# Kernel tuning notes

Measured on AMD Instinct MI355X. Metric: run time of the kernel, lower is better.

## Reference

```python
import jax, jax.numpy as jnp
import numpy as np

B, S, CC, CF, E, H, NH = 16, 1024, 8, 8, 64, 1024, 16
DH = H // NH
VOCAB = 10000
EPS = 1e-5


def layer_norm(x, g, b):
    m = x.mean(-1, keepdims=True)
    v = x.var(-1, keepdims=True)
    return (x - m) / jnp.sqrt(v + EPS) * g + b


def setup_inputs():
    key = jax.random.key(0)
    ks = jax.random.split(key, 30)
    f32 = jnp.float32
    n = lambda k, shp, s=0.02: jax.random.normal(k, shp, f32) * s
    inp = {}
    inp['cate_x'] = jax.random.randint(ks[0], (B, S, CC), 0, VOCAB)
    inp['cont_x'] = jax.random.normal(ks[1], (B, S, CF), f32)
    inp['mask'] = jax.random.randint(ks[2], (B, S), 0, 2)
    # parameters
    inp['emb_table'] = n(ks[3], (VOCAB, E)).at[0].set(0.0)  # padding_idx=0
    inp['cate_W'] = n(ks[4], (CC * E, H)); inp['cate_b'] = jnp.zeros((H,), f32)
    inp['cate_ln_g'] = jnp.ones((H,), f32); inp['cate_ln_b'] = jnp.zeros((H,), f32)
    inp['bn_g'] = jnp.ones((CF,), f32); inp['bn_b'] = jnp.zeros((CF,), f32)
    inp['cont_W'] = n(ks[5], (CF, H)); inp['cont_b'] = jnp.zeros((H,), f32)
    inp['cont_ln_g'] = jnp.ones((H,), f32); inp['cont_ln_b'] = jnp.zeros((H,), f32)
    inp['comb_W'] = n(ks[6], (2 * H, H)); inp['comb_b'] = jnp.zeros((H,), f32)
    inp['comb_ln_g'] = jnp.ones((H,), f32); inp['comb_ln_b'] = jnp.zeros((H,), f32)
    inp['Wq'] = n(ks[7], (H, H)); inp['bq'] = jnp.zeros((H,), f32)
    inp['Wk'] = n(ks[8], (H, H)); inp['bk'] = jnp.zeros((H,), f32)
    inp['Wv'] = n(ks[9], (H, H)); inp['bv'] = jnp.zeros((H,), f32)
    inp['Wo'] = n(ks[10], (H, H)); inp['bo'] = jnp.zeros((H,), f32)
    return inp


def reference(cate_x, cont_x, mask, emb_table, cate_W, cate_b, cate_ln_g, cate_ln_b,
              bn_g, bn_b, cont_W, cont_b, cont_ln_g, cont_ln_b,
              comb_W, comb_b, comb_ln_g, comb_ln_b,
              Wq, bq, Wk, bk, Wv, bv, Wo, bo):
    # categorical path: embed -> flatten cols -> Linear+LN
    cate_emb = emb_table[cate_x].reshape(B, S, CC * E)
    cate_h = layer_norm(cate_emb @ cate_W + cate_b, cate_ln_g, cate_ln_b)
    # continuous path: BatchNorm1d over flattened (B*S, CF) with batch stats
    xf = cont_x.reshape(-1, CF)
    mu = xf.mean(0)
    var = xf.var(0)  # biased, as torch BN normalization
    xn = ((xf - mu) / jnp.sqrt(var + EPS) * bn_g + bn_b).reshape(B, S, CF)
    cont_h = layer_norm(xn @ cont_W + cont_b, cont_ln_g, cont_ln_b)
    # combine: ReLU -> Linear -> LN
    seq = jax.nn.relu(jnp.concatenate([cate_h, cont_h], axis=2))
    x = layer_norm(seq @ comb_W + comb_b, comb_ln_g, comb_ln_b)  # [B,S,H]
    # multi-head attention (dropout is identity in eval)
    Q = (x @ Wq + bq).reshape(B, S, NH, DH)
    K = (x @ Wk + bk).reshape(B, S, NH, DH)
    V = (x @ Wv + bv).reshape(B, S, NH, DH)
    scores = jnp.einsum('bqhd,bkhd->bhqk', Q, K) / np.sqrt(DH).astype(np.float32)
    # faithful to source: mask broadcast over the QUERY axis
    scores = jnp.where(mask[:, None, :, None] == 0, -1e7, scores)
    attn = jax.nn.softmax(scores, axis=-1)
    out = jnp.einsum('bhqk,bkhd->bqhd', attn, V).reshape(B, S, H)
    out = out @ Wo + bo
    return out[:, -1:, -1]  # [B,1]
```

## Files before the change

kernel.cpp:

```cpp
#include <hip/hip_runtime.h>
#include <hip/hip_bf16.h>
#include <math.h>

#define EPS 1e-5f

typedef unsigned short u16;
typedef __attribute__((ext_vector_type(8))) short bf16x8;
typedef __attribute__((ext_vector_type(4))) float f32x4;

__device__ __forceinline__ float b2f(u16 u) {
  union { unsigned int i; float f; } v; v.i = ((unsigned int)u) << 16; return v.f;
}
__device__ __forceinline__ u16 f2b(float f) {
  union { float f; unsigned int i; } v; v.f = f;
  unsigned int r = v.i + 0x7fff + ((v.i >> 16) & 1);
  return (u16)(r >> 16);
}

__device__ __forceinline__ void gload_lds16(const u16* g, u16* l) {
  __builtin_amdgcn_global_load_lds(
      (const __attribute__((address_space(1))) unsigned int*)g,
      (__attribute__((address_space(3))) unsigned int*)l, 16, 0, 0);
}

__global__ __launch_bounds__(256) void prep_k(
    const float* __restrict__ cx, float* __restrict__ part_bn,
    float* __restrict__ outacc,
    const float* __restrict__ emb, u16* __restrict__ embb,
    const float* __restrict__ cate_W, u16* __restrict__ cateWT) {
  __shared__ float shmem[64 * 65];
  const int bid = blockIdx.x, tid = threadIdx.x;

  if (bid == 0) {
    if (tid < 16) outacc[tid] = 0.f;
    return;
  }
  if (bid <= 64) {
    int pb = bid - 1;
    int gid = pb * 256 + tid;
    float4 a = ((const float4*)cx)[2 * gid];
    float4 b = ((const float4*)cx)[2 * gid + 1];
    float v[16];
    v[0] = a.x; v[1] = a.y; v[2] = a.z; v[3] = a.w;
    v[4] = b.x; v[5] = b.y; v[6] = b.z; v[7] = b.w;
#pragma unroll
    for (int i = 0; i < 8; ++i) v[8 + i] = v[i] * v[i];
#pragma unroll
    for (int off = 32; off; off >>= 1)
#pragma unroll
      for (int i = 0; i < 16; ++i) v[i] += __shfl_down(v[i], off);
    int l = tid & 63, wv_ = tid >> 6;
    if (l == 0)
#pragma unroll
      for (int i = 0; i < 16; ++i) shmem[wv_ * 16 + i] = v[i];
    __syncthreads();
    if (tid < 16)
      part_bn[pb * 16 + tid] = shmem[tid] + shmem[16 + tid] + shmem[32 + tid] + shmem[48 + tid];
    return;
  }
  if (bid <= 689) {
    int i = (bid - 65) * 256 + tid;
    if (i < 160000) {
      float4 v = ((const float4*)emb)[i];
      ushort4 u; u.x = f2b(v.x); u.y = f2b(v.y); u.z = f2b(v.z); u.w = f2b(v.w);
      ((ushort4*)embb)[i] = u;
    }
    return;
  }
  {
    int local = bid - 690;
    int n0 = (local & 15) * 64, k0 = (local >> 4) * 64;
    int c = tid & 63, r0 = tid >> 6;
#pragma unroll
    for (int i = 0; i < 16; ++i) {
      int r = r0 + i * 4;
      shmem[r * 65 + c] = cate_W[(size_t)(k0 + r) * 1024 + n0 + c];
    }
    __syncthreads();
#pragma unroll
    for (int i = 0; i < 16; ++i) {
      int r = r0 + i * 4;
      cateWT[(size_t)(n0 + r) * 512 + k0 + c] = f2b(shmem[c * 65 + r]);
    }
  }
}

template <int MODE>
__global__ __launch_bounds__(512) void gemm256(
    const u16* __restrict__ A0, const u16* __restrict__ A1,
    const int* __restrict__ idx, const u16* __restrict__ embb,
    const u16* __restrict__ BT, const float* __restrict__ bias,
    u16* __restrict__ C, int K) {
  __shared__ u16 As[2][2][8192];
  __shared__ u16 Bs[2][2][8192];
  __shared__ int sidx[MODE == 1 ? 2048 : 4];
  const int tid = threadIdx.x;
  const int bid = blockIdx.x;
  const int col0 = (bid & 3) * 256;
  const int row0 = ((((bid >> 2) & 1) << 5) + (bid >> 3)) * 256;

  const int rr8 = tid >> 3;
  const int p8  = tid & 7;
  const int sl  = p8 ^ (rr8 & 7);

  const int l   = tid & 63;
  const int w   = tid >> 6;
  const int wrh = w >> 2;
  const int wcq = w & 3;
  const int hb  = wcq >> 1;
  const int rbb = (wcq & 1) * 64;
  const int lr  = l & 15;
  const int lk  = l >> 4;

  f32x4 acc[8][4];
#pragma unroll
  for (int m = 0; m < 8; ++m)
#pragma unroll
    for (int n = 0; n < 4; ++n) acc[m][n] = (f32x4){0.f, 0.f, 0.f, 0.f};

  const int nt = K >> 6;
  const int nit = nt >> 1;

  if (MODE == 1) {
    *(int4*)&sidx[tid * 4] = *(const int4*)&idx[row0 * 8 + tid * 4];
    __syncthreads();
  }

  auto stageA = [&](int t, int h) {
    const int k0 = t << 6;
    const int buf = t & 1;
#pragma unroll
    for (int i = 0; i < 2; ++i) {
      const u16* asrc;
      if (MODE == 1) {
        int id = sidx[(h * 128 + i * 64 + rr8) * 8 + (k0 >> 6)];
        asrc = embb + (size_t)id * 64 + sl * 8;
      } else {
        int ar = row0 + h * 128 + i * 64 + rr8;
        const u16* base = (k0 < 1024) ? A0 : A1;
        asrc = base + (size_t)ar * 1024 + (k0 & 1023) + sl * 8;
      }
      gload_lds16(asrc, &As[buf][h][i * 4096 + tid * 8]);
    }
  };
  auto stageB = [&](int t, int h) {
    const int k0 = t << 6;
    const int buf = t & 1;
#pragma unroll
    for (int i = 0; i < 2; ++i) {
      int br = col0 + h * 128 + i * 64 + rr8;
      gload_lds16(BT + (size_t)br * K + k0 + sl * 8,
                  &Bs[buf][h][i * 4096 + tid * 8]);
    }
  };

  bf16x8 bfr[4][2];
  auto loadB = [&](int buf) {
#pragma unroll
    for (int n = 0; n < 4; ++n)
#pragma unroll
      for (int ks = 0; ks < 2; ++ks) {
        int rowb = rbb + n * 16 + lr;
        int ph = (ks * 4 + lk) ^ (lr & 7);
        bfr[n][ks] = *(const bf16x8*)&Bs[buf][hb][rowb * 64 + ph * 8];
      }
  };
  auto loadA = [&](bf16x8 (&af)[2][2], int buf, int q) {
#pragma unroll
    for (int mm = 0; mm < 2; ++mm)
#pragma unroll
      for (int ks = 0; ks < 2; ++ks) {
        int rowa = (q * 2 + mm) * 16 + lr;
        int ph = (ks * 4 + lk) ^ (lr & 7);
        af[mm][ks] = *(const bf16x8*)&As[buf][wrh][rowa * 64 + ph * 8];
      }
  };
  auto mfma_quad = [&](bf16x8 (&af)[2][2], int q) {
    __builtin_amdgcn_s_setprio(1);
#pragma unroll
    for (int ks = 0; ks < 2; ++ks)
#pragma unroll
      for (int mm = 0; mm < 2; ++mm)
#pragma unroll
        for (int n = 0; n < 4; ++n)
          acc[q * 2 + mm][n] = __builtin_amdgcn_mfma_f32_16x16x32_bf16(
              af[mm][ks], bfr[n][ks], acc[q * 2 + mm][n], 0, 0, 0);
    __builtin_amdgcn_s_setprio(0);
  };

  stageA(0, 0); stageA(0, 1);
  stageB(0, 0); stageB(0, 1);
  stageB(1, 0); stageB(1, 1);
  asm volatile("s_waitcnt vmcnt(4)" ::: "memory");
  __builtin_amdgcn_s_barrier();

  for (int it = 0; it < nit; ++it) {
    const int T = it * 2;
    const bool more = (T + 2 < nt);
    bf16x8 af[2][2];

    loadB(0); loadA(af, 0, 0);
    stageA(T + 1, 0);
    __builtin_amdgcn_s_barrier();
    asm volatile("s_waitcnt lgkmcnt(0)" ::: "memory");
    mfma_quad(af, 0);
    __builtin_amdgcn_s_barrier();
    loadA(af, 0, 1);
    stageA(T + 1, 1);
    __builtin_amdgcn_s_barrier();
    asm volatile("s_waitcnt lgkmcnt(0)" ::: "memory");
    mfma_quad(af, 1);
    __builtin_amdgcn_s_barrier();
    loadA(af, 0, 2);
    if (more) stageB(T + 2, 0);
    __builtin_amdgcn_s_barrier();
    asm volatile("s_waitcnt lgkmcnt(0)" ::: "memory");
    mfma_quad(af, 2);
    __builtin_amdgcn_s_barrier();
    loadA(af, 0, 3);
    if (more) stageB(T + 2, 1);
    __builtin_amdgcn_s_barrier();
    asm volatile("s_waitcnt lgkmcnt(0)" ::: "memory");
    mfma_quad(af, 3);
    if (more) asm volatile("s_waitcnt vmcnt(4)" ::: "memory");
    else      asm volatile("s_waitcnt vmcnt(0)" ::: "memory");
    __builtin_amdgcn_s_barrier();

    loadB(1); loadA(af, 1, 0);
    if (more) stageA(T + 2, 0);
    __builtin_amdgcn_s_barrier();
    asm volatile("s_waitcnt lgkmcnt(0)" ::: "memory");
    mfma_quad(af, 0);
    __builtin_amdgcn_s_barrier();
    loadA(af, 1, 1);
    if (more) stageA(T + 2, 1);
    __builtin_amdgcn_s_barrier();
    asm volatile("s_waitcnt lgkmcnt(0)" ::: "memory");
    mfma_quad(af, 1);
    __builtin_amdgcn_s_barrier();
    loadA(af, 1, 2);
    if (more) stageB(T + 3, 0);
    __builtin_amdgcn_s_barrier();
    asm volatile("s_waitcnt lgkmcnt(0)" ::: "memory");
    mfma_quad(af, 2);
    __builtin_amdgcn_s_barrier();
    loadA(af, 1, 3);
    if (more) stageB(T + 3, 1);
    __builtin_amdgcn_s_barrier();
    asm volatile("s_waitcnt lgkmcnt(0)" ::: "memory");
    mfma_quad(af, 3);
    if (it + 1 < nit) {
      asm volatile("s_waitcnt vmcnt(4)" ::: "memory");
      __builtin_amdgcn_s_barrier();
    }
  }

  float bv_[4];
#pragma unroll
  for (int n = 0; n < 4; ++n) bv_[n] = bias[col0 + wcq * 64 + n * 16 + lr];
#pragma unroll
  for (int m = 0; m < 8; ++m) {
#pragma unroll
    for (int n = 0; n < 4; ++n) {
      int cc = col0 + wcq * 64 + n * 16 + lr;
#pragma unroll
      for (int q4 = 0; q4 < 4; ++q4) {
        int rr = row0 + wrh * 128 + m * 16 + lk * 4 + q4;
        C[(size_t)rr * 1024 + cc] = f2b(acc[m][n][q4] + bv_[n]);
      }
    }
  }
}

__device__ __forceinline__ void ln_body(u16* __restrict__ buf,
                                        const float* __restrict__ g,
                                        const float* __restrict__ b, int relu,
                                        int blk, int tid) {
  int lane = tid & 63, wave = tid >> 6;
  size_t row = (size_t)blk * 4 + wave;
  u16* p = buf + row * 1024 + lane * 16;
  uint4 u0 = *(uint4*)p;
  uint4 u1 = *(uint4*)(p + 8);
  float x[16];
#pragma unroll
  for (int i = 0; i < 4; ++i) {
    unsigned int w0 = ((unsigned int*)&u0)[i];
    unsigned int w1 = ((unsigned int*)&u1)[i];
    x[2 * i]     = b2f((u16)(w0 & 0xffff));
    x[2 * i + 1] = b2f((u16)(w0 >> 16));
    x[8 + 2 * i]     = b2f((u16)(w1 & 0xffff));
    x[8 + 2 * i + 1] = b2f((u16)(w1 >> 16));
  }
  float s = 0.f, s2 = 0.f;
#pragma unroll
  for (int i = 0; i < 16; ++i) { s += x[i]; s2 += x[i] * x[i]; }
#pragma unroll
  for (int off = 32; off; off >>= 1) { s += __shfl_xor(s, off); s2 += __shfl_xor(s2, off); }
  float mean = s * (1.f / 1024.f);
  float var = s2 * (1.f / 1024.f) - mean * mean;
  float rs = rsqrtf(var + EPS);
  float y[16];
#pragma unroll
  for (int q = 0; q < 4; ++q) {
    float4 gv = *(const float4*)(g + lane * 16 + q * 4);
    float4 bv = *(const float4*)(b + lane * 16 + q * 4);
    y[4 * q]     = (x[4 * q]     - mean) * rs * gv.x + bv.x;
    y[4 * q + 1] = (x[4 * q + 1] - mean) * rs * gv.y + bv.y;
    y[4 * q + 2] = (x[4 * q + 2] - mean) * rs * gv.z + bv.z;
    y[4 * q + 3] = (x[4 * q + 3] - mean) * rs * gv.w + bv.w;
  }
  if (relu)
#pragma unroll
    for (int i = 0; i < 16; ++i) y[i] = fmaxf(y[i], 0.f);
  uint4 o0, o1;
#pragma unroll
  for (int i = 0; i < 4; ++i) {
    ((unsigned int*)&o0)[i] = (unsigned int)f2b(y[2 * i]) | ((unsigned int)f2b(y[2 * i + 1]) << 16);
    ((unsigned int*)&o1)[i] = (unsigned int)f2b(y[8 + 2 * i]) | ((unsigned int)f2b(y[8 + 2 * i + 1]) << 16);
  }
  *(uint4*)p = o0;
  *(uint4*)(p + 8) = o1;
}

__global__ __launch_bounds__(256) void ln_k(u16* __restrict__ buf,
                                            const float* __restrict__ g,
                                            const float* __restrict__ b, int relu) {
  ln_body(buf, g, b, relu, blockIdx.x, threadIdx.x);
}

__device__ __forceinline__ void cont_body(const float* __restrict__ cx,
                                          const float* __restrict__ part_bn,
                                          const float* __restrict__ bn_g,
                                          const float* __restrict__ bn_b,
                                          const float* __restrict__ W,
                                          const float* __restrict__ cb,
                                          const float* __restrict__ g,
                                          const float* __restrict__ bb,
                                          u16* __restrict__ out,
                                          int row0, int tid) {
  __shared__ float sp[4][16];
  __shared__ float tt[16];
  __shared__ float ab[2][8];
  __shared__ float xn[8][8];
  __shared__ float rr1[4][8], rr2[4][8];

  if (tid < 64) {
    int f = tid & 15, qd = tid >> 4;
    float s = 0.f;
    for (int j = qd * 16; j < qd * 16 + 16; ++j) s += part_bn[j * 16 + f];
    sp[qd][f] = s;
  }
  __syncthreads();
  if (tid < 16) tt[tid] = sp[0][tid] + sp[1][tid] + sp[2][tid] + sp[3][tid];
  __syncthreads();
  if (tid < 8) {
    float mu = tt[tid] * (1.f / 16384.f);
    float var = tt[8 + tid] * (1.f / 16384.f) - mu * mu;
    float a = rsqrtf(var + EPS) * bn_g[tid];
    ab[0][tid] = a;
    ab[1][tid] = bn_b[tid] - mu * a;
  }
  __syncthreads();
  if (tid < 64) {
    int r = tid >> 3, f = tid & 7;
    xn[r][f] = ab[0][f] * cx[(row0 + r) * 8 + f] + ab[1][f];
  }
  __syncthreads();

  int c = tid * 4;
  float4 cbv = *(const float4*)(cb + c);
  float acc[8][4];
#pragma unroll
  for (int r = 0; r < 8; ++r) {
    acc[r][0] = cbv.x; acc[r][1] = cbv.y; acc[r][2] = cbv.z; acc[r][3] = cbv.w;
  }
  for (int k = 0; k < 8; ++k) {
    float4 w4 = *(const float4*)(W + k * 1024 + c);
#pragma unroll
    for (int r = 0; r < 8; ++r) {
      float xv = xn[r][k];
      acc[r][0] = fmaf(xv, w4.x, acc[r][0]);
      acc[r][1] = fmaf(xv, w4.y, acc[r][1]);
      acc[r][2] = fmaf(xv, w4.z, acc[r][2]);
      acc[r][3] = fmaf(xv, w4.w, acc[r][3]);
    }
  }
  float s1[8], s2[8];
#pragma unroll
  for (int r = 0; r < 8; ++r) {
    s1[r] = acc[r][0] + acc[r][1] + acc[r][2] + acc[r][3];
    s2[r] = acc[r][0] * acc[r][0] + acc[r][1] * acc[r][1] +
            acc[r][2] * acc[r][2] + acc[r][3] * acc[r][3];
  }
#pragma unroll
  for (int off = 32; off; off >>= 1)
#pragma unroll
    for (int r = 0; r < 8; ++r) {
      s1[r] += __shfl_down(s1[r], off);
      s2[r] += __shfl_down(s2[r], off);
    }
  int lane = tid & 63, wv = tid >> 6;
  if (lane == 0)
#pragma unroll
    for (int r = 0; r < 8; ++r) { rr1[wv][r] = s1[r]; rr2[wv][r] = s2[r]; }
  __syncthreads();
  float4 gv = *(const float4*)(g + c);
  float4 bv = *(const float4*)(bb + c);
#pragma unroll
  for (int r = 0; r < 8; ++r) {
    float ss = rr1[0][r] + rr1[1][r] + rr1[2][r] + rr1[3][r];
    float qq = rr2[0][r] + rr2[1][r] + rr2[2][r] + rr2[3][r];
    float mean = ss * (1.f / 1024.f);
    float var = qq * (1.f / 1024.f) - mean * mean;
    float rs = rsqrtf(var + EPS);
    float y0 = fmaxf((acc[r][0] - mean) * rs * gv.x + bv.x, 0.f);
    float y1 = fmaxf((acc[r][1] - mean) * rs * gv.y + bv.y, 0.f);
    float y2 = fmaxf((acc[r][2] - mean) * rs * gv.z + bv.z, 0.f);
    float y3 = fmaxf((acc[r][3] - mean) * rs * gv.w + bv.w, 0.f);
    ushort4 o; o.x = f2b(y0); o.y = f2b(y1); o.z = f2b(y2); o.w = f2b(y3);
    *(ushort4*)(out + (size_t)(row0 + r) * 1024 + c) = o;
  }
}

__global__ __launch_bounds__(256) void mid_k(
    u16* __restrict__ X1, const float* __restrict__ cate_g,
    const float* __restrict__ cate_bb,
    const float* __restrict__ comb_W, u16* __restrict__ combWT,
    const float* __restrict__ Wv, const float* __restrict__ Wo,
    float* __restrict__ wvo,
    const float* __restrict__ cx, const float* __restrict__ part_bn,
    const float* __restrict__ bn_g, const float* __restrict__ bn_b,
    const float* __restrict__ cont_W, const float* __restrict__ cont_b,
    const float* __restrict__ cont_g, const float* __restrict__ cont_bb,
    u16* __restrict__ X2) {
  __shared__ float shmem[64 * 65];
  const int bid = blockIdx.x, tid = threadIdx.x;
  if (bid < 4096) {
    ln_body(X1, cate_g, cate_bb, 1, bid, tid);
    return;
  }
  if (bid < 4608) {
    int local = bid - 4096;
    int n0 = (local & 15) * 64, k0 = (local >> 4) * 64;
    int c = tid & 63, r0 = tid >> 6;
#pragma unroll
    for (int i = 0; i < 16; ++i) {
      int r = r0 + i * 4;
      shmem[r * 65 + c] = comb_W[(size_t)(k0 + r) * 1024 + n0 + c];
    }
    __syncthreads();
#pragma unroll
    for (int i = 0; i < 16; ++i) {
      int r = r0 + i * 4;
      combWT[(size_t)(n0 + r) * 2048 + k0 + c] = f2b(shmem[c * 65 + r]);
    }
    return;
  }
  if (bid < 4672) {
    int local = bid - 4608;
    int h = local >> 2, jc = local & 3;
    if (tid < 64) shmem[tid] = Wo[(size_t)(h * 64 + tid) * 1024 + 1023];
    __syncthreads();
    int j = jc * 256 + tid;
    const float* vr = Wv + (size_t)j * 1024 + h * 64;
    float s = 0.f;
    for (int d4 = 0; d4 < 64; d4 += 4) {
      float4 w4 = *(const float4*)(vr + d4);
      s = fmaf(w4.x, shmem[d4], s);
      s = fmaf(w4.y, shmem[d4 + 1], s);
      s = fmaf(w4.z, shmem[d4 + 2], s);
      s = fmaf(w4.w, shmem[d4 + 3], s);
    }
    wvo[h * 1024 + j] = s;
    return;
  }
  {
    int row0 = (bid - 4672) * 8;
    cont_body(cx, part_bn, bn_g, bn_b, cont_W, cont_b, cont_g, cont_bb, X2,
              row0, tid);
  }
}

__global__ __launch_bounds__(256) void qproj_k(const u16* __restrict__ x,
                                               const float* __restrict__ Wq,
                                               const float* __restrict__ bq,
                                               float* __restrict__ q) {
  __shared__ u16 xs[16][1024];
  __shared__ float part[16][16][16];
  int tid = threadIdx.x;
  for (int i = tid; i < 4096; i += 256) {
    int b = i >> 8, off = (i & 255) * 4;
    *(ushort4*)&xs[b][off] =
        *(const ushort4*)(x + ((size_t)(b * 1024 + 1023)) * 1024 + off);
  }
  __syncthreads();
  int c = tid & 15;
  int col = blockIdx.x * 16 + c;
  int kq = tid >> 4;
  float acc[16];
#pragma unroll
  for (int b = 0; b < 16; ++b) acc[b] = 0.f;
  for (int k = kq * 64; k < kq * 64 + 64; ++k) {
    float wv = Wq[(size_t)k * 1024 + col];
#pragma unroll
    for (int b = 0; b < 16; ++b) acc[b] = fmaf(b2f(xs[b][k]), wv, acc[b]);
  }
#pragma unroll
  for (int b = 0; b < 16; ++b) part[kq][b][c] = acc[b];
  __syncthreads();
  if (tid < 256) {
    int b = tid >> 4, cc = tid & 15;
    float s = 0.f;
#pragma unroll
    for (int j = 0; j < 16; ++j) s += part[j][b][cc];
    q[b * 1024 + blockIdx.x * 16 + cc] = s + bq[blockIdx.x * 16 + cc];
  }
}

__global__ __launch_bounds__(256) void kq_k(const float* __restrict__ Wk,
                                            const float* __restrict__ bk,
                                            const float* __restrict__ q,
                                            u16* __restrict__ qtb,
                                            float* __restrict__ bkq) {
  int h = blockIdx.x >> 2, jc = blockIdx.x & 3;
  int tid = threadIdx.x;
  __shared__ float Qs[16][64];
  for (int i = tid; i < 1024; i += 256) {
    int b = i >> 6, d = i & 63;
    Qs[b][d] = q[b * 1024 + h * 64 + d];
  }
  __syncthreads();
  int j = jc * 256 + tid;
  float acc[16];
#pragma unroll
  for (int b = 0; b < 16; ++b) acc[b] = 0.f;
  const float* wr = Wk + (size_t)j * 1024 + h * 64;
  for (int d4 = 0; d4 < 64; d4 += 4) {
    float4 w4 = *(const float4*)(wr + d4);
#pragma unroll
    for (int b = 0; b < 16; ++b) {
      acc[b] = fmaf(w4.x, Qs[b][d4], acc[b]);
      acc[b] = fmaf(w4.y, Qs[b][d4 + 1], acc[b]);
      acc[b] = fmaf(w4.z, Qs[b][d4 + 2], acc[b]);
      acc[b] = fmaf(w4.w, Qs[b][d4 + 3], acc[b]);
    }
  }
#pragma unroll
  for (int b = 0; b < 16; ++b) qtb[((size_t)b * 16 + h) * 1024 + j] = f2b(acc[b]);
  if (jc == 0 && tid < 16) {
    int b = tid;
    float s = 0.f;
    for (int d = 0; d < 64; ++d) s = fmaf(bk[h * 64 + d], Qs[b][d], s);
    bkq[b * 16 + h] = s;
  }
}

__global__ __launch_bounds__(256) void score_k(const u16* __restrict__ x,
                                               const u16* __restrict__ qtb,
                                               const float* __restrict__ bkq,
                                               const int* __restrict__ mask,
                                               float* __restrict__ sc) {
  int b = blockIdx.x >> 4, kc = blockIdx.x & 15;
  int tid = threadIdx.x;
  int l = tid & 63, w = tid >> 6;
  int keybase = kc * 64 + w * 16;
  int lr = l & 15, ls = l >> 4;
  int masked = (mask[b * 1024 + 1023] == 0);

  f32x4 acc = (f32x4){0.f, 0.f, 0.f, 0.f};
  const u16* xb = x + (size_t)b * 1024 * 1024;
  const u16* qb = qtb + (size_t)b * 16 * 1024;
  for (int k0 = 0; k0 < 1024; k0 += 32) {
    bf16x8 bfr = *(const bf16x8*)&qb[(size_t)lr * 1024 + k0 + ls * 8];
    bf16x8 afr = *(const bf16x8*)&xb[(size_t)(keybase + lr) * 1024 + k0 + ls * 8];
    acc = __builtin_amdgcn_mfma_f32_16x16x32_bf16(afr, bfr, acc, 0, 0, 0);
  }
  int h = lr;
  float bq_ = bkq[b * 16 + h];
#pragma unroll
  for (int q = 0; q < 4; ++q) {
    int key = keybase + ls * 4 + q;
    float v = masked ? 0.f : (acc[q] + bq_) * 0.125f;
    sc[((size_t)b * 16 + h) * 1024 + key] = v;
  }
}

__global__ __launch_bounds__(256) void attnw_k(float* __restrict__ sc) {
  int bh = blockIdx.x, tid = threadIdx.x;
  float* row = sc + (size_t)bh * 1024;
  float4 v = ((float4*)row)[tid];
  float m = fmaxf(fmaxf(v.x, v.y), fmaxf(v.z, v.w));
#pragma unroll
  for (int off = 32; off; off >>= 1) m = fmaxf(m, __shfl_down(m, off));
  __shared__ float rm[4], rs_[4];
  int lane = tid & 63, wv = tid >> 6;
  if (lane == 0) rm[wv] = m;
  __syncthreads();
  m = fmaxf(fmaxf(rm[0], rm[1]), fmaxf(rm[2], rm[3]));
  float e0 = expf(v.x - m), e1 = expf(v.y - m), e2 = expf(v.z - m), e3 = expf(v.w - m);
  float s = e0 + e1 + e2 + e3;
#pragma unroll
  for (int off = 32; off; off >>= 1) s += __shfl_down(s, off);
  if (lane == 0) rs_[wv] = s;
  __syncthreads();
  s = rs_[0] + rs_[1] + rs_[2] + rs_[3];
  float inv = 1.f / s;
  float4 o; o.x = e0 * inv; o.y = e1 * inv; o.z = e2 * inv; o.w = e3 * inv;
  ((float4*)row)[tid] = o;
}

__global__ __launch_bounds__(256) void ctx_k(const float* __restrict__ p,
                                             const u16* __restrict__ x,
                                             const float* __restrict__ wvo,
                                             float* __restrict__ outacc) {
  int b = blockIdx.x >> 4, kc = blockIdx.x & 15;
  int tid = threadIdx.x;
  __shared__ float pl[64][16];
  for (int i = tid; i < 1024; i += 256) {
    int kk = i >> 4, hh = i & 15;
    pl[kk][hh] = p[((size_t)b * 16 + hh) * 1024 + kc * 64 + kk];
  }
  __syncthreads();
  float acc[16][4];
#pragma unroll
  for (int h = 0; h < 16; ++h)
#pragma unroll
    for (int j = 0; j < 4; ++j) acc[h][j] = 0.f;
  const u16* xb = x + ((size_t)(b * 1024 + kc * 64)) * 1024 + tid * 4;
  for (int k = 0; k < 64; ++k) {
    ushort4 u = *(const ushort4*)(xb + (size_t)k * 1024);
    float x0 = b2f(u.x), x1 = b2f(u.y), x2 = b2f(u.z), x3 = b2f(u.w);
#pragma unroll
    for (int h4 = 0; h4 < 4; ++h4) {
      float4 pv = *(const float4*)&pl[k][h4 * 4];
      acc[h4 * 4 + 0][0] = fmaf(pv.x, x0, acc[h4 * 4 + 0][0]);
      acc[h4 * 4 + 0][1] = fmaf(pv.x, x1, acc[h4 * 4 + 0][1]);
      acc[h4 * 4 + 0][2] = fmaf(pv.x, x2, acc[h4 * 4 + 0][2]);
      acc[h4 * 4 + 0][3] = fmaf(pv.x, x3, acc[h4 * 4 + 0][3]);
      acc[h4 * 4 + 1][0] = fmaf(pv.y, x0, acc[h4 * 4 + 1][0]);
      acc[h4 * 4 + 1][1] = fmaf(pv.y, x1, acc[h4 * 4 + 1][1]);
      acc[h4 * 4 + 1][2] = fmaf(pv.y, x2, acc[h4 * 4 + 1][2]);
      acc[h4 * 4 + 1][3] = fmaf(pv.y, x3, acc[h4 * 4 + 1][3]);
      acc[h4 * 4 + 2][0] = fmaf(pv.z, x0, acc[h4 * 4 + 2][0]);
      acc[h4 * 4 + 2][1] = fmaf(pv.z, x1, acc[h4 * 4 + 2][1]);
      acc[h4 * 4 + 2][2] = fmaf(pv.z, x2, acc[h4 * 4 + 2][2]);
      acc[h4 * 4 + 2][3] = fmaf(pv.z, x3, acc[h4 * 4 + 2][3]);
      acc[h4 * 4 + 3][0] = fmaf(pv.w, x0, acc[h4 * 4 + 3][0]);
      acc[h4 * 4 + 3][1] = fmaf(pv.w, x1, acc[h4 * 4 + 3][1]);
      acc[h4 * 4 + 3][2] = fmaf(pv.w, x2, acc[h4 * 4 + 3][2]);
      acc[h4 * 4 + 3][3] = fmaf(pv.w, x3, acc[h4 * 4 + 3][3]);
    }
  }
  float s = 0.f;
#pragma unroll
  for (int h = 0; h < 16; ++h) {
    float4 w4 = *(const float4*)&wvo[h * 1024 + tid * 4];
    s += acc[h][0] * w4.x + acc[h][1] * w4.y + acc[h][2] * w4.z + acc[h][3] * w4.w;
  }
#pragma unroll
  for (int off = 32; off; off >>= 1) s += __shfl_down(s, off);
  __shared__ float r[4];
  int lane = tid & 63, wv = tid >> 6;
  if (lane == 0) r[wv] = s;
  __syncthreads();
  if (tid == 0) atomicAdd(&outacc[b], r[0] + r[1] + r[2] + r[3]);
}

__global__ __launch_bounds__(256) void bfinal_k(const float* __restrict__ outacc,
                                                const float* __restrict__ bv,
                                                const float* __restrict__ Wo,
                                                const float* __restrict__ bo,
                                                float* __restrict__ out) {
  int tid = threadIdx.x;
  float s = 0.f;
  for (int i = tid; i < 1024; i += 256) s = fmaf(bv[i], Wo[(size_t)i * 1024 + 1023], s);
#pragma unroll
  for (int off = 32; off; off >>= 1) s += __shfl_down(s, off);
  __shared__ float r[4];
  int lane = tid & 63, wv = tid >> 6;
  if (lane == 0) r[wv] = s;
  __syncthreads();
  float bc = r[0] + r[1] + r[2] + r[3] + bo[1023];
  if (tid < 16) out[tid] = outacc[tid] + bc;
}

extern "C" void kernel_launch(void* const* d_in, const int* in_sizes, int n_in,
                              void* d_out, int out_size, void* d_ws, size_t ws_size,
                              hipStream_t stream) {
  const int*   cate_x  = (const int*)d_in[0];
  const float* cont_x  = (const float*)d_in[1];
  const int*   mask    = (const int*)d_in[2];
  const float* emb     = (const float*)d_in[3];
  const float* cate_W  = (const float*)d_in[4];
  const float* cate_b  = (const float*)d_in[5];
  const float* cate_g  = (const float*)d_in[6];
  const float* cate_bb = (const float*)d_in[7];
  const float* bn_g    = (const float*)d_in[8];
  const float* bn_b    = (const float*)d_in[9];
  const float* cont_W  = (const float*)d_in[10];
  const float* cont_b  = (const float*)d_in[11];
  const float* cont_g  = (const float*)d_in[12];
  const float* cont_bb = (const float*)d_in[13];
  const float* Wq = (const float*)d_in[18]; const float* bq = (const float*)d_in[19];
  const float* Wk = (const float*)d_in[20]; const float* bk = (const float*)d_in[21];
  const float* Wv = (const float*)d_in[22]; const float* bv = (const float*)d_in[23];
  const float* Wo = (const float*)d_in[24]; const float* bo = (const float*)d_in[25];
  const float* comb_W  = (const float*)d_in[14];
  const float* comb_b  = (const float*)d_in[15];
  const float* comb_g  = (const float*)d_in[16];
  const float* comb_bb = (const float*)d_in[17];
  float* out = (float*)d_out;

  char* w = (char*)d_ws;
  float* stats   = (float*)w;
  float* outacc  = stats + 16;
  float* part_bn = (float*)(w + 256);
  float* qbuf    = (float*)(w + 8192);
  u16* embb      = (u16*)(w + 131328);
  u16* cateWT    = (u16*)(w + 1411328);
  u16* combWT    = (u16*)(w + 2459904);
  float* sc      = (float*)(w + 6654208);
  u16*   qtb     = (u16*)(w + 7702784);
  float* wvo     = (float*)(w + 8227072);
  float* bkq     = (float*)(w + 8292608);
  u16* X1        = (u16*)(w + 10848512);
  u16* X2        = X1 + (size_t)16777216;
  u16* xb        = X2 + (size_t)16777216;

  prep_k<<<818, 256, 0, stream>>>(cont_x, part_bn, outacc, emb, embb,
                                  cate_W, cateWT);

  gemm256<1><<<256, 512, 0, stream>>>(nullptr, nullptr, cate_x, embb, cateWT,
                                      cate_b, X1, 512);
  mid_k<<<6720, 256, 0, stream>>>(X1, cate_g, cate_bb, comb_W, combWT, Wv, Wo,
                                  wvo, cont_x, part_bn, bn_g, bn_b, cont_W,
                                  cont_b, cont_g, cont_bb, X2);
  gemm256<2><<<256, 512, 0, stream>>>(X1, X2, nullptr, nullptr, combWT,
                                      comb_b, xb, 2048);
  ln_k<<<4096, 256, 0, stream>>>(xb, comb_g, comb_bb, 0);

  qproj_k<<<64, 256, 0, stream>>>(xb, Wq, bq, qbuf);
  kq_k<<<64, 256, 0, stream>>>(Wk, bk, qbuf, qtb, bkq);
  score_k<<<256, 256, 0, stream>>>(xb, qtb, bkq, mask, sc);
  attnw_k<<<256, 256, 0, stream>>>(sc);
  ctx_k<<<256, 256, 0, stream>>>(sc, xb, wvo, outacc);
  bfinal_k<<<1, 256, 0, stream>>>(outacc, bv, Wo, bo, out);
}
```

Before: 213.8 us.

## Fold value-output projection into score pass and replace context kernel

Computes per-key projections y = x·(Wv·Wo[:,last]) per head with MFMA inside the score kernel, using a split hi/lo bf16 representation to preserve precision. The softmax kernel then reduces exp-weighted y directly, so the separate normalization write and the ctx_k pass that re-read the full activation tensor are removed. It also changes the GEMM block-to-tile mapping to a different swizzle. The cost is two extra MFMAs per step in score_k and an extra y buffer.

```diff
diff --git a/kernel.cpp b/kernel.cpp
--- a/kernel.cpp
+++ b/kernel.cpp
@@ -96,8 +96,10 @@
   __shared__ int sidx[MODE == 1 ? 2048 : 4];
   const int tid = threadIdx.x;
   const int bid = blockIdx.x;
-  const int col0 = (bid & 3) * 256;
-  const int row0 = ((((bid >> 2) & 1) << 5) + (bid >> 3)) * 256;
+  const int chunk = gridDim.x >> 3;
+  const int swz = (bid & 7) * chunk + (bid >> 3);
+  const int row0 = (swz >> 2) * 256;
+  const int col0 = (swz & 3) * 256;
 
   const int rr8 = tid >> 3;
   const int p8  = tid & 7;
@@ -427,7 +429,8 @@
     const float* __restrict__ cate_bb,
     const float* __restrict__ comb_W, u16* __restrict__ combWT,
     const float* __restrict__ Wv, const float* __restrict__ Wo,
-    float* __restrict__ wvo,
+    u16* __restrict__ wvob_hi, u16* __restrict__ wvob_lo,
+    float* __restrict__ woc,
     const float* __restrict__ cx, const float* __restrict__ part_bn,
     const float* __restrict__ bn_g, const float* __restrict__ bn_b,
     const float* __restrict__ cont_W, const float* __restrict__ cont_b,
@@ -461,6 +464,7 @@
     int h = local >> 2, jc = local & 3;
     if (tid < 64) shmem[tid] = Wo[(size_t)(h * 64 + tid) * 1024 + 1023];
     __syncthreads();
+    if (jc == 0 && tid < 64) woc[h * 64 + tid] = shmem[tid];
     int j = jc * 256 + tid;
     const float* vr = Wv + (size_t)j * 1024 + h * 64;
     float s = 0.f;
@@ -471,7 +475,10 @@
       s = fmaf(w4.z, shmem[d4 + 2], s);
       s = fmaf(w4.w, shmem[d4 + 3], s);
     }
-    wvo[h * 1024 + j] = s;
+    u16 hi = f2b(s);
+    float lo = s - b2f(hi);
+    wvob_hi[h * 1024 + j] = hi;
+    wvob_lo[h * 1024 + j] = f2b(lo);
     return;
   }
   {
@@ -559,7 +566,10 @@
                                                const u16* __restrict__ qtb,
                                                const float* __restrict__ bkq,
                                                const int* __restrict__ mask,
-                                               float* __restrict__ sc) {
+                                               const u16* __restrict__ whi,
+                                               const u16* __restrict__ wlo,
+                                               float* __restrict__ sc,
+                                               float* __restrict__ y) {
   int b = blockIdx.x >> 4, kc = blockIdx.x & 15;
   int tid = threadIdx.x;
   int l = tid & 63, w = tid >> 6;
@@ -568,12 +578,17 @@
   int masked = (mask[b * 1024 + 1023] == 0);
 
   f32x4 acc = (f32x4){0.f, 0.f, 0.f, 0.f};
+  f32x4 acy = (f32x4){0.f, 0.f, 0.f, 0.f};
   const u16* xb = x + (size_t)b * 1024 * 1024;
   const u16* qb = qtb + (size_t)b * 16 * 1024;
   for (int k0 = 0; k0 < 1024; k0 += 32) {
     bf16x8 bfr = *(const bf16x8*)&qb[(size_t)lr * 1024 + k0 + ls * 8];
+    bf16x8 bh  = *(const bf16x8*)&whi[(size_t)lr * 1024 + k0 + ls * 8];
+    bf16x8 bl  = *(const bf16x8*)&wlo[(size_t)lr * 1024 + k0 + ls * 8];
     bf16x8 afr = *(const bf16x8*)&xb[(size_t)(keybase + lr) * 1024 + k0 + ls * 8];
     acc = __builtin_amdgcn_mfma_f32_16x16x32_bf16(afr, bfr, acc, 0, 0, 0);
+    acy = __builtin_amdgcn_mfma_f32_16x16x32_bf16(afr, bh, acy, 0, 0, 0);
+    acy = __builtin_amdgcn_mfma_f32_16x16x32_bf16(afr, bl, acy, 0, 0, 0);
   }
   int h = lr;
   float bq_ = bkq[b * 16 + h];
@@ -582,98 +597,49 @@
     int key = keybase + ls * 4 + q;
     float v = masked ? 0.f : (acc[q] + bq_) * 0.125f;
     sc[((size_t)b * 16 + h) * 1024 + key] = v;
-  }
-}
-
-__global__ __launch_bounds__(256) void attnw_k(float* __restrict__ sc) {
+    y[((size_t)b * 16 + h) * 1024 + key] = acy[q];
+  }
+}
+
+__global__ __launch_bounds__(256) void fin_k(const float* __restrict__ sc,
+                                             const float* __restrict__ y,
+                                             float* __restrict__ outacc) {
   int bh = blockIdx.x, tid = threadIdx.x;
-  float* row = sc + (size_t)bh * 1024;
-  float4 v = ((float4*)row)[tid];
+  float4 v = ((const float4*)(sc + (size_t)bh * 1024))[tid];
   float m = fmaxf(fmaxf(v.x, v.y), fmaxf(v.z, v.w));
 #pragma unroll
   for (int off = 32; off; off >>= 1) m = fmaxf(m, __shfl_down(m, off));
-  __shared__ float rm[4], rs_[4];
+  __shared__ float rm[4], rs_[4], rd_[4];
   int lane = tid & 63, wv = tid >> 6;
   if (lane == 0) rm[wv] = m;
   __syncthreads();
   m = fmaxf(fmaxf(rm[0], rm[1]), fmaxf(rm[2], rm[3]));
   float e0 = expf(v.x - m), e1 = expf(v.y - m), e2 = expf(v.z - m), e3 = expf(v.w - m);
+  float4 yv = ((const float4*)(y + (size_t)bh * 1024))[tid];
   float s = e0 + e1 + e2 + e3;
-#pragma unroll
-  for (int off = 32; off; off >>= 1) s += __shfl_down(s, off);
-  if (lane == 0) rs_[wv] = s;
-  __syncthreads();
-  s = rs_[0] + rs_[1] + rs_[2] + rs_[3];
-  float inv = 1.f / s;
-  float4 o; o.x = e0 * inv; o.y = e1 * inv; o.z = e2 * inv; o.w = e3 * inv;
-  ((float4*)row)[tid] = o;
-}
-
-__global__ __launch_bounds__(256) void ctx_k(const float* __restrict__ p,
-                                             const u16* __restrict__ x,
-                                             const float* __restrict__ wvo,
-                                             float* __restrict__ outacc) {
-  int b = blockIdx.x >> 4, kc = blockIdx.x & 15;
-  int tid = threadIdx.x;
-  __shared__ float pl[64][16];
-  for (int i = tid; i < 1024; i += 256) {
-    int kk = i >> 4, hh = i & 15;
-    pl[kk][hh] = p[((size_t)b * 16 + hh) * 1024 + kc * 64 + kk];
-  }
-  __syncthreads();
-  float acc[16][4];
-#pragma unroll
-  for (int h = 0; h < 16; ++h)
-#pragma unroll
-    for (int j = 0; j < 4; ++j) acc[h][j] = 0.f;
-  const u16* xb = x + ((size_t)(b * 1024 + kc * 64)) * 1024 + tid * 4;
-  for (int k = 0; k < 64; ++k) {
-    ushort4 u = *(const ushort4*)(xb + (size_t)k * 1024);
-    float x0 = b2f(u.x), x1 = b2f(u.y), x2 = b2f(u.z), x3 = b2f(u.w);
-#pragma unroll
-    for (int h4 = 0; h4 < 4; ++h4) {
-      float4 pv = *(const float4*)&pl[k][h4 * 4];
-      acc[h4 * 4 + 0][0] = fmaf(pv.x, x0, acc[h4 * 4 + 0][0]);
-      acc[h4 * 4 + 0][1] = fmaf(pv.x, x1, acc[h4 * 4 + 0][1]);
-      acc[h4 * 4 + 0][2] = fmaf(pv.x, x2, acc[h4 * 4 + 0][2]);
-      acc[h4 * 4 + 0][3] = fmaf(pv.x, x3, acc[h4 * 4 + 0][3]);
-      acc[h4 * 4 + 1][0] = fmaf(pv.y, x0, acc[h4 * 4 + 1][0]);
-      acc[h4 * 4 + 1][1] = fmaf(pv.y, x1, acc[h4 * 4 + 1][1]);
-      acc[h4 * 4 + 1][2] = fmaf(pv.y, x2, acc[h4 * 4 + 1][2]);
-      acc[h4 * 4 + 1][3] = fmaf(pv.y, x3, acc[h4 * 4 + 1][3]);
-      acc[h4 * 4 + 2][0] = fmaf(pv.z, x0, acc[h4 * 4 + 2][0]);
-      acc[h4 * 4 + 2][1] = fmaf(pv.z, x1, acc[h4 * 4 + 2][1]);
-      acc[h4 * 4 + 2][2] = fmaf(pv.z, x2, acc[h4 * 4 + 2][2]);
-      acc[h4 * 4 + 2][3] = fmaf(pv.z, x3, acc[h4 * 4 + 2][3]);
-      acc[h4 * 4 + 3][0] = fmaf(pv.w, x0, acc[h4 * 4 + 3][0]);
-      acc[h4 * 4 + 3][1] = fmaf(pv.w, x1, acc[h4 * 4 + 3][1]);
-      acc[h4 * 4 + 3][2] = fmaf(pv.w, x2, acc[h4 * 4 + 3][2]);
-      acc[h4 * 4 + 3][3] = fmaf(pv.w, x3, acc[h4 * 4 + 3][3]);
-    }
-  }
-  float s = 0.f;
-#pragma unroll
-  for (int h = 0; h < 16; ++h) {
-    float4 w4 = *(const float4*)&wvo[h * 1024 + tid * 4];
-    s += acc[h][0] * w4.x + acc[h][1] * w4.y + acc[h][2] * w4.z + acc[h][3] * w4.w;
-  }
-#pragma unroll
-  for (int off = 32; off; off >>= 1) s += __shfl_down(s, off);
-  __shared__ float r[4];
-  int lane = tid & 63, wv = tid >> 6;
-  if (lane == 0) r[wv] = s;
-  __syncthreads();
-  if (tid == 0) atomicAdd(&outacc[b], r[0] + r[1] + r[2] + r[3]);
+  float d = e0 * yv.x + e1 * yv.y + e2 * yv.z + e3 * yv.w;
+#pragma unroll
+  for (int off = 32; off; off >>= 1) {
+    s += __shfl_down(s, off);
+    d += __shfl_down(d, off);
+  }
+  if (lane == 0) { rs_[wv] = s; rd_[wv] = d; }
+  __syncthreads();
+  if (tid == 0) {
+    float Z = rs_[0] + rs_[1] + rs_[2] + rs_[3];
+    float D = rd_[0] + rd_[1] + rd_[2] + rd_[3];
+    atomicAdd(&outacc[bh >> 4], D / Z);
+  }
 }
 
 __global__ __launch_bounds__(256) void bfinal_k(const float* __restrict__ outacc,
                                                 const float* __restrict__ bv,
-                                                const float* __restrict__ Wo,
+                                                const float* __restrict__ woc,
                                                 const float* __restrict__ bo,
                                                 float* __restrict__ out) {
   int tid = threadIdx.x;
   float s = 0.f;
-  for (int i = tid; i < 1024; i += 256) s = fmaf(bv[i], Wo[(size_t)i * 1024 + 1023], s);
+  for (int i = tid; i < 1024; i += 256) s = fmaf(bv[i], woc[i], s);
 #pragma unroll
   for (int off = 32; off; off >>= 1) s += __shfl_down(s, off);
   __shared__ float r[4];
@@ -721,8 +687,11 @@
   u16* combWT    = (u16*)(w + 2459904);
   float* sc      = (float*)(w + 6654208);
   u16*   qtb     = (u16*)(w + 7702784);
-  float* wvo     = (float*)(w + 8227072);
   float* bkq     = (float*)(w + 8292608);
+  float* ybuf    = (float*)(w + 8388608);
+  u16* wvob_hi   = (u16*)(w + 9437184);
+  u16* wvob_lo   = (u16*)(w + 9469952);
+  float* woc     = (float*)(w + 9502720);
   u16* X1        = (u16*)(w + 10848512);
   u16* X2        = X1 + (size_t)16777216;
   u16* xb        = X2 + (size_t)16777216;
@@ -733,16 +702,15 @@
   gemm256<1><<<256, 512, 0, stream>>>(nullptr, nullptr, cate_x, embb, cateWT,
                                       cate_b, X1, 512);
   mid_k<<<6720, 256, 0, stream>>>(X1, cate_g, cate_bb, comb_W, combWT, Wv, Wo,
-                                  wvo, cont_x, part_bn, bn_g, bn_b, cont_W,
-                                  cont_b, cont_g, cont_bb, X2);
+                                  wvob_hi, wvob_lo, woc, cont_x, part_bn, bn_g,
+                                  bn_b, cont_W, cont_b, cont_g, cont_bb, X2);
   gemm256<2><<<256, 512, 0, stream>>>(X1, X2, nullptr, nullptr, combWT,
                                       comb_b, xb, 2048);
   ln_k<<<4096, 256, 0, stream>>>(xb, comb_g, comb_bb, 0);
 
   qproj_k<<<64, 256, 0, stream>>>(xb, Wq, bq, qbuf);
   kq_k<<<64, 256, 0, stream>>>(Wk, bk, qbuf, qtb, bkq);
-  score_k<<<256, 256, 0, stream>>>(xb, qtb, bkq, mask, sc);
-  attnw_k<<<256, 256, 0, stream>>>(sc);
-  ctx_k<<<256, 256, 0, stream>>>(sc, xb, wvo, outacc);
-  bfinal_k<<<1, 256, 0, stream>>>(outacc, bv, Wo, bo, out);
-}
+  score_k<<<256, 256, 0, stream>>>(xb, qtb, bkq, mask, wvob_hi, wvob_lo, sc, ybuf);
+  fin_k<<<256, 256, 0, stream>>>(sc, ybuf, outacc);
+  bfinal_k<<<1, 256, 0, stream>>>(outacc, bv, woc, bo, out);
+}
```

Measured after the change: 198.7 us. -7.1%, faster.
